# Kernel tuning notes

Measured on AMD Instinct MI355X. Metric: run time of the kernel, lower is better.

Reference implementation:

```python
import jax, jax.numpy as jnp
import numpy as np

B, LQ, LKV, D = 32, 1024, 1024, 512

def setup_inputs() -> dict:
    key = jax.random.key(0)
    kq, kkv = jax.random.split(key)
    query = jax.random.normal(kq, (B, LQ, D), dtype=jnp.float32)
    key_value = jax.random.normal(kkv, (B, LKV, D), dtype=jnp.float32)
    return {"query": query, "key_value": key_value}

def reference(query, key_value):
    # scores: [B, Lq, Lkv] (unscaled dot-product attention)
    scores = jnp.einsum('bqd,bkd->bqk', query, key_value)
    attn_score = jax.nn.softmax(scores, axis=-1)
    # output: [B, Lq, D]
    output = jnp.einsum('bqk,bkd->bqd', attn_score, key_value)
    return (output, attn_score)
```

## Files before the change

kernel.cpp:

```cpp
#include <hip/hip_runtime.h>


constexpr int NB  = 32;
constexpr int LQ  = 1024;
constexpr int LKV = 1024;
constexpr int DD  = 512;
constexpr int NROWS = NB * LQ;

typedef __attribute__((ext_vector_type(4))) float f4;
typedef __attribute__((ext_vector_type(4))) float f32x4;
typedef __attribute__((ext_vector_type(4))) unsigned short u16x4;
typedef __attribute__((ext_vector_type(8))) __bf16 bf16x8;

__device__ __forceinline__ unsigned short f2bf(float x) {
  unsigned u = __builtin_bit_cast(unsigned, x);
  unsigned r = u + 0x7FFFu + ((u >> 16) & 1u);
  return (unsigned short)(r >> 16);
}
__device__ __forceinline__ float bf2f(unsigned short h) {
  unsigned u = ((unsigned)h) << 16;
  return __builtin_bit_cast(float, u);
}

__device__ __forceinline__ void gload16(const void* g, void* l) {
  __builtin_amdgcn_global_load_lds((const __attribute__((address_space(1))) unsigned int*)g,
                                   (__attribute__((address_space(3))) unsigned int*)l,
                                   16, 0, 0);
}

constexpr int PAD = 40;

__global__ __launch_bounds__(256) void prep_all_kernel(const float* __restrict__ Q,
                                                       const float* __restrict__ KV,
                                                       unsigned short* __restrict__ Qh,
                                                       unsigned short* __restrict__ Ql,
                                                       unsigned short* __restrict__ Kh,
                                                       unsigned short* __restrict__ Kl,
                                                       unsigned short* __restrict__ KVT)
{
  __shared__ unsigned short T[64][72];
  const int b  = blockIdx.z;
  const int tk = blockIdx.y;
  const int td = blockIdx.x;
  const int tid = threadIdx.x;

#pragma unroll
  for (int i = 0; i < 4; ++i) {
    int idx = tid + i * 256;
    int r   = idx >> 4;
    int c4  = (idx & 15) << 2;
    size_t goff = ((size_t)b * LKV + tk * 64 + r) * DD + td * 64 + c4;
    f4 v = *(const f4*)(KV + goff);
    u16x4 h, l;
#pragma unroll
    for (int u = 0; u < 4; ++u) {
      h[u] = f2bf(v[u]);
      l[u] = f2bf(v[u] - bf2f(h[u]));
    }
    *(u16x4*)&T[r][c4] = h;
    *(u16x4*)(Kh + goff) = h;
    *(u16x4*)(Kl + goff) = l;

    f4 q = *(const f4*)(Q + goff);
    u16x4 qh, ql;
#pragma unroll
    for (int u = 0; u < 4; ++u) {
      qh[u] = f2bf(q[u]);
      ql[u] = f2bf(q[u] - bf2f(qh[u]));
    }
    *(u16x4*)(Qh + goff) = qh;
    *(u16x4*)(Ql + goff) = ql;
  }
  __syncthreads();

#pragma unroll
  for (int i = 0; i < 4; ++i) {
    int idx = tid + i * 256;
    int c   = idx >> 4;
    int r4  = (idx & 15) << 2;
    u16x4 w = { T[r4][c], T[r4 + 1][c], T[r4 + 2][c], T[r4 + 3][c] };
    *(u16x4*)(KVT + ((size_t)b * DD + td * 64 + c) * LKV + tk * 64 + r4) = w;
  }
}

__global__ __launch_bounds__(256) void gemm_qk4_kernel(const unsigned short* __restrict__ Qh,
                                                       const unsigned short* __restrict__ Ql,
                                                       const unsigned short* __restrict__ Kh,
                                                       const unsigned short* __restrict__ Kl,
                                                       float* __restrict__ S,
                                                       float* __restrict__ Pmax,
                                                       float* __restrict__ Psum)
{
  __shared__ unsigned short SM[4][128 * 64];
  const int b   = blockIdx.y;
  const int ti  = blockIdx.x >> 3;
  const int tj  = blockIdx.x & 7;
  const int tid  = threadIdx.x;
  const int lane = tid & 63;
  const int wid  = tid >> 6;
  const int wr = (wid >> 1) * 64;
  const int wc = (wid & 1) * 64;

  const size_t qo = ((size_t)b * LQ  + ti * 128) * DD;
  const size_t ko = ((size_t)b * LKV + tj * 128) * DD;
  const unsigned short* tb =
      (wid == 0) ? Qh + qo : (wid == 1) ? Ql + qo : (wid == 2) ? Kh + ko : Kl + ko;

  const int lrow = lane >> 3;
  const int ss   = (lane & 7) ^ lrow;

  f32x4 acc[4][4] = {};

  for (int ks = 0; ks < DD; ks += 64) {
    __syncthreads();
#pragma unroll
    for (int i = 0; i < 16; ++i) {
      const unsigned short* g = tb + (size_t)(i * 8 + lrow) * DD + ks + ss * 8;
      gload16(g, &SM[wid][i * 512]);
    }
    __syncthreads();

#pragma unroll
    for (int kk = 0; kk < 64; kk += 32) {
      const int cl  = (kk + ((lane >> 4) << 3)) >> 3;
      const int sp8 = (cl ^ (lane & 7)) * 8;
      bf16x8 ah[4], al[4], bh[4], bl[4];
#pragma unroll
      for (int m = 0; m < 4; ++m) {
        int r = wr + m * 16 + (lane & 15);
        ah[m] = *(const bf16x8*)&SM[0][r * 64 + sp8];
        al[m] = *(const bf16x8*)&SM[1][r * 64 + sp8];
      }
#pragma unroll
      for (int n = 0; n < 4; ++n) {
        int r = wc + n * 16 + (lane & 15);
        bh[n] = *(const bf16x8*)&SM[2][r * 64 + sp8];
        bl[n] = *(const bf16x8*)&SM[3][r * 64 + sp8];
      }
#pragma unroll
      for (int m = 0; m < 4; ++m)
#pragma unroll
        for (int n = 0; n < 4; ++n)
          acc[m][n] = __builtin_amdgcn_mfma_f32_16x16x32_bf16(ah[m], bh[n], acc[m][n], 0, 0, 0);
#pragma unroll
      for (int m = 0; m < 4; ++m)
#pragma unroll
        for (int n = 0; n < 4; ++n)
          acc[m][n] = __builtin_amdgcn_mfma_f32_16x16x32_bf16(ah[m], bl[n], acc[m][n], 0, 0, 0);
#pragma unroll
      for (int m = 0; m < 4; ++m)
#pragma unroll
        for (int n = 0; n < 4; ++n)
          acc[m][n] = __builtin_amdgcn_mfma_f32_16x16x32_bf16(al[m], bh[n], acc[m][n], 0, 0, 0);
    }
  }

  float* Sb = S + (size_t)b * LQ * LKV;
#pragma unroll
  for (int m = 0; m < 4; ++m) {
    int row0 = ti * 128 + wr + m * 16 + ((lane >> 4) << 2);
#pragma unroll
    for (int n = 0; n < 4; ++n) {
      int col = tj * 128 + wc + n * 16 + (lane & 15);
#pragma unroll
      for (int j = 0; j < 4; ++j)
        Sb[(size_t)(row0 + j) * LKV + col] = acc[m][n][j];
    }
  }

  const int g16  = lane >> 4;
  const int l16  = lane & 15;
  const int wcid = wc >> 6;
#pragma unroll
  for (int m = 0; m < 4; ++m) {
#pragma unroll
    for (int j = 0; j < 4; ++j) {
      float rm = fmaxf(fmaxf(acc[m][0][j], acc[m][1][j]), fmaxf(acc[m][2][j], acc[m][3][j]));
#pragma unroll
      for (int off = 8; off >= 1; off >>= 1)
        rm = fmaxf(rm, __shfl_xor(rm, off));
      float se = 0.f;
#pragma unroll
      for (int n = 0; n < 4; ++n)
        se += __expf(acc[m][n][j] - rm);
#pragma unroll
      for (int off = 8; off >= 1; off >>= 1)
        se += __shfl_xor(se, off);
      if (l16 == 0) {
        int row  = ti * 128 + wr + m * 16 + g16 * 4 + j;
        size_t p = ((size_t)b * LQ + row) * 16 + tj * 2 + wcid;
        Pmax[p] = rm;
        Psum[p] = se;
      }
    }
  }
}

__global__ __launch_bounds__(256) void reduce_stats_kernel(const float* __restrict__ Pmax,
                                                           const float* __restrict__ Psum,
                                                           float* __restrict__ M,
                                                           float* __restrict__ Inv)
{
  int row = blockIdx.x * 256 + threadIdx.x;
  const float* pm = Pmax + (size_t)row * 16;
  const float* ps = Psum + (size_t)row * 16;
  float mx = pm[0];
#pragma unroll
  for (int i = 1; i < 16; ++i) mx = fmaxf(mx, pm[i]);
  float s = 0.f;
#pragma unroll
  for (int i = 0; i < 16; ++i) s += ps[i] * __expf(pm[i] - mx);
  M[row]   = mx;
  Inv[row] = 1.0f / s;
}

__global__ __launch_bounds__(1024, 4) void gemm_av7_kernel(float* __restrict__ Sio,
                                                           const unsigned short* __restrict__ KVT,
                                                           const float* __restrict__ Mrow,
                                                           const float* __restrict__ Invr,
                                                           float* __restrict__ O)
{
  __shared__ unsigned short Asm[128][72];
  __shared__ unsigned short Bsm[512 * 64];
  __shared__ float Ms[128], Is[128];
  const int b  = blockIdx.y;
  const int mi = blockIdx.x;
  const int tid  = threadIdx.x;
  const int lane = tid & 63;
  const int wid  = tid >> 6;
  const int wr  = (wid >> 2) * 32;
  const int wcb = (wid & 3) * 128;

  float* Sb = Sio + ((size_t)b * LQ + mi * 128) * LKV;
  const unsigned short* Bb = KVT + (size_t)b * DD * LKV;

  if (tid < 128) {
    int gr = b * LQ + mi * 128 + tid;
    Ms[tid] = Mrow[gr];
    Is[tid] = Invr[gr];
  }

  const int lr8 = lane >> 3;
  const int ssw = (lane & 7) ^ lr8;

  f32x4 acc[2][8] = {};

  for (int ks = 0; ks < LKV; ks += 64) {
    __syncthreads();
#pragma unroll
    for (int i = 0; i < 2; ++i) {
      int idx = tid + i * 1024;
      int r   = idx >> 4;
      int k4  = (idx & 15) << 2;
      float* ap = Sb + (size_t)r * LKV + ks + k4;
      f4 v = *(const f4*)ap;
      float mr = Ms[r], ir = Is[r];
      f4 p; u16x4 h;
#pragma unroll
      for (int u = 0; u < 4; ++u) {
        p[u] = __expf(v[u] - mr) * ir;
        h[u] = f2bf(p[u]);
      }
      *(f4*)ap = p;
      *(u16x4*)&Asm[r][k4] = h;
    }
#pragma unroll
    for (int c = 0; c < 4; ++c) {
      int cc = wid * 4 + c;
      int dd = cc * 8 + lr8;
      const unsigned short* g = Bb + (size_t)dd * LKV + ks + ssw * 8;
      gload16(g, &Bsm[cc * 512]);
    }
    __syncthreads();

#pragma unroll
    for (int kk = 0; kk < 64; kk += 32) {
      const int kf = kk + ((lane >> 4) << 3);
      const int cl = kf >> 3;
      bf16x8 af[2];
#pragma unroll
      for (int m = 0; m < 2; ++m)
        af[m] = *(const bf16x8*)&Asm[wr + m * 16 + (lane & 15)][kf];
#pragma unroll
      for (int h = 0; h < 2; ++h) {
        bf16x8 bfv[4];
#pragma unroll
        for (int nn = 0; nn < 4; ++nn) {
          int dd = wcb + (h * 4 + nn) * 16 + (lane & 15);
          int sp = cl ^ (dd & 7);
          bfv[nn] = *(const bf16x8*)&Bsm[dd * 64 + sp * 8];
        }
#pragma unroll
        for (int m = 0; m < 2; ++m)
#pragma unroll
          for (int nn = 0; nn < 4; ++nn)
            acc[m][h * 4 + nn] =
                __builtin_amdgcn_mfma_f32_16x16x32_bf16(af[m], bfv[nn], acc[m][h * 4 + nn], 0, 0, 0);
      }
    }
  }

  float* Ob = O + ((size_t)b * LQ + mi * 128) * DD;
#pragma unroll
  for (int m = 0; m < 2; ++m) {
    int r0 = wr + m * 16 + ((lane >> 4) << 2);
#pragma unroll
    for (int n = 0; n < 8; ++n) {
      int col = wcb + n * 16 + (lane & 15);
#pragma unroll
      for (int j = 0; j < 4; ++j)
        Ob[(size_t)(r0 + j) * DD + col] = acc[m][n][j];
    }
  }
}

__global__ __launch_bounds__(256) void gemm_qk_kernel(const float* __restrict__ Q,
                                                      const float* __restrict__ KV,
                                                      float* __restrict__ S)
{
  __shared__ unsigned short Ah[128][PAD], Al[128][PAD], Bh[128][PAD], Bl[128][PAD];
  const int b   = blockIdx.y;
  const int ti  = blockIdx.x >> 3;
  const int tj  = blockIdx.x & 7;
  const int tid  = threadIdx.x;
  const int lane = tid & 63;
  const int wid  = tid >> 6;
  const int wr = (wid >> 1) * 64;
  const int wc = (wid & 1) * 64;

  const float* Qb = Q  + (size_t)b * LQ  * DD + (size_t)ti * 128 * DD;
  const float* Kb = KV + (size_t)b * LKV * DD + (size_t)tj * 128 * DD;

  f32x4 acc[4][4] = {};

  for (int ks = 0; ks < DD; ks += 32) {
    __syncthreads();
#pragma unroll
    for (int i = 0; i < 4; ++i) {
      int idx = tid + i * 256;
      int r   = idx >> 3;
      int k4  = (idx & 7) << 2;
      f4 qa = *(const f4*)(Qb + (size_t)r * DD + ks + k4);
      f4 ka = *(const f4*)(Kb + (size_t)r * DD + ks + k4);
      u16x4 qh, ql, kh, kl;
#pragma unroll
      for (int u = 0; u < 4; ++u) {
        unsigned short h = f2bf(qa[u]);
        qh[u] = h;  ql[u] = f2bf(qa[u] - bf2f(h));
        unsigned short h2 = f2bf(ka[u]);
        kh[u] = h2; kl[u] = f2bf(ka[u] - bf2f(h2));
      }
      *(u16x4*)&Ah[r][k4] = qh;  *(u16x4*)&Al[r][k4] = ql;
      *(u16x4*)&Bh[r][k4] = kh;  *(u16x4*)&Bl[r][k4] = kl;
    }
    __syncthreads();

    const int kf = (lane >> 4) << 3;
    bf16x8 ah[4], al[4], bh[4], bl[4];
#pragma unroll
    for (int m = 0; m < 4; ++m) {
      int row = wr + m * 16 + (lane & 15);
      ah[m] = *(const bf16x8*)&Ah[row][kf];
      al[m] = *(const bf16x8*)&Al[row][kf];
    }
#pragma unroll
    for (int n = 0; n < 4; ++n) {
      int row = wc + n * 16 + (lane & 15);
      bh[n] = *(const bf16x8*)&Bh[row][kf];
      bl[n] = *(const bf16x8*)&Bl[row][kf];
    }
#pragma unroll
    for (int m = 0; m < 4; ++m)
#pragma unroll
      for (int n = 0; n < 4; ++n) {
        acc[m][n] = __builtin_amdgcn_mfma_f32_16x16x32_bf16(ah[m], bh[n], acc[m][n], 0, 0, 0);
        acc[m][n] = __builtin_amdgcn_mfma_f32_16x16x32_bf16(ah[m], bl[n], acc[m][n], 0, 0, 0);
        acc[m][n] = __builtin_amdgcn_mfma_f32_16x16x32_bf16(al[m], bh[n], acc[m][n], 0, 0, 0);
      }
  }

  float* Sb = S + (size_t)b * LQ * LKV;
#pragma unroll
  for (int m = 0; m < 4; ++m) {
    int row0 = ti * 128 + wr + m * 16 + ((lane >> 4) << 2);
#pragma unroll
    for (int n = 0; n < 4; ++n) {
      int col = tj * 128 + wc + n * 16 + (lane & 15);
#pragma unroll
      for (int j = 0; j < 4; ++j)
        Sb[(size_t)(row0 + j) * LKV + col] = acc[m][n][j];
    }
  }
}

__global__ __launch_bounds__(256) void softmax_kernel(float* __restrict__ S)
{
  __shared__ float redmax[4], redsum[4];
  const int tid = threadIdx.x;
  float* p = S + (size_t)blockIdx.x * LKV;

  f4 v = *(const f4*)(p + tid * 4);
  float mx = fmaxf(fmaxf(v[0], v[1]), fmaxf(v[2], v[3]));
#pragma unroll
  for (int off = 32; off >= 1; off >>= 1)
    mx = fmaxf(mx, __shfl_xor(mx, off));
  if ((tid & 63) == 0) redmax[tid >> 6] = mx;
  __syncthreads();
  mx = fmaxf(fmaxf(redmax[0], redmax[1]), fmaxf(redmax[2], redmax[3]));

  f4 e;
#pragma unroll
  for (int u = 0; u < 4; ++u) e[u] = __expf(v[u] - mx);
  float sm = e[0] + e[1] + e[2] + e[3];
#pragma unroll
  for (int off = 32; off >= 1; off >>= 1)
    sm += __shfl_xor(sm, off);
  if ((tid & 63) == 0) redsum[tid >> 6] = sm;
  __syncthreads();
  sm = redsum[0] + redsum[1] + redsum[2] + redsum[3];

  float inv = 1.0f / sm;
  f4 o = { e[0] * inv, e[1] * inv, e[2] * inv, e[3] * inv };
  *(f4*)(p + tid * 4) = o;
}

__global__ __launch_bounds__(256) void kvt_prep_kernel(const float* __restrict__ KV,
                                                       unsigned short* __restrict__ KVT)
{
  __shared__ unsigned short T[64][72];
  const int b  = blockIdx.z;
  const int tk = blockIdx.y;
  const int td = blockIdx.x;
  const int tid = threadIdx.x;

#pragma unroll
  for (int i = 0; i < 4; ++i) {
    int idx = tid + i * 256;
    int r   = idx >> 4;
    int c4  = (idx & 15) << 2;
    f4 v = *(const f4*)(KV + ((size_t)b * LKV + tk * 64 + r) * DD + td * 64 + c4);
    u16x4 h;
#pragma unroll
    for (int u = 0; u < 4; ++u) h[u] = f2bf(v[u]);
    *(u16x4*)&T[r][c4] = h;
  }
  __syncthreads();

#pragma unroll
  for (int i = 0; i < 4; ++i) {
    int idx = tid + i * 256;
    int c   = idx >> 4;
    int r4  = (idx & 15) << 2;
    u16x4 w = { T[r4][c], T[r4 + 1][c], T[r4 + 2][c], T[r4 + 3][c] };
    *(u16x4*)(KVT + ((size_t)b * DD + td * 64 + c) * LKV + tk * 64 + r4) = w;
  }
}

__global__ __launch_bounds__(512) void gemm_av2_kernel(const float* __restrict__ A,
                                                       const unsigned short* __restrict__ KVT,
                                                       float* __restrict__ O)
{
  __shared__ unsigned short Asm[128][72];
  __shared__ unsigned short Bsm[256 * 64];
  const int b  = blockIdx.z;
  const int mi = blockIdx.y;
  const int nj = blockIdx.x;
  const int tid  = threadIdx.x;
  const int lane = tid & 63;
  const int wid  = tid >> 6;
  const int wr = (wid >> 2) * 64;
  const int wc = (wid & 3) * 64;

  const float* Ab = A + (size_t)b * LQ * LKV + (size_t)mi * 128 * LKV;
  const unsigned short* Bb = KVT + ((size_t)b * DD + nj * 256) * LKV;

  f32x4 acc[4][4] = {};

  for (int ks = 0; ks < LKV; ks += 64) {
    __syncthreads();
#pragma unroll
    for (int i = 0; i < 4; ++i) {
      int idx = tid + i * 512;
      int r   = idx >> 4;
      int k4  = (idx & 15) << 2;
      f4 v = *(const f4*)(Ab + (size_t)r * LKV + ks + k4);
      u16x4 h;
#pragma unroll
      for (int u = 0; u < 4; ++u) h[u] = f2bf(v[u]);
      *(u16x4*)&Asm[r][k4] = h;
    }
#pragma unroll
    for (int c = 0; c < 4; ++c) {
      int cc = wid * 4 + c;
      int dd = cc * 8 + (lane >> 3);
      int ss = (lane & 7) ^ (dd & 7);
      const unsigned short* g = Bb + (size_t)dd * LKV + ks + ss * 8;
      gload16(g, &Bsm[cc * 512]);
    }
    __syncthreads();

#pragma unroll
    for (int kk = 0; kk < 64; kk += 32) {
      const int kf = kk + ((lane >> 4) << 3);
      const int cl = kf >> 3;
      bf16x8 af[4], bfv[4];
#pragma unroll
      for (int m = 0; m < 4; ++m)
        af[m] = *(const bf16x8*)&Asm[wr + m * 16 + (lane & 15)][kf];
#pragma unroll
      for (int n = 0; n < 4; ++n) {
        int dd = wc + n * 16 + (lane & 15);
        int sp = cl ^ (dd & 7);
        bfv[n] = *(const bf16x8*)&Bsm[dd * 64 + sp * 8];
      }
#pragma unroll
      for (int m = 0; m < 4; ++m)
#pragma unroll
        for (int n = 0; n < 4; ++n)
          acc[m][n] = __builtin_amdgcn_mfma_f32_16x16x32_bf16(af[m], bfv[n], acc[m][n], 0, 0, 0);
    }
  }

  float* Ob = O + (size_t)b * LQ * DD;
#pragma unroll
  for (int m = 0; m < 4; ++m) {
    int row0 = mi * 128 + wr + m * 16 + ((lane >> 4) << 2);
#pragma unroll
    for (int n = 0; n < 4; ++n) {
      int col = nj * 256 + wc + n * 16 + (lane & 15);
#pragma unroll
      for (int j = 0; j < 4; ++j)
        Ob[(size_t)(row0 + j) * DD + col] = acc[m][n][j];
    }
  }
}

__global__ __launch_bounds__(256) void gemm_av_kernel(const float* __restrict__ A,
                                                      const float* __restrict__ KV,
                                                      float* __restrict__ O)
{
  __shared__ unsigned short Ab[128][PAD], Bt[128][PAD];
  const int b  = blockIdx.z;
  const int mi = blockIdx.y;
  const int nj = blockIdx.x;
  const int tid  = threadIdx.x;
  const int lane = tid & 63;
  const int wid  = tid >> 6;
  const int wr = (wid >> 1) * 64;
  const int wc = (wid & 1) * 64;

  const float* Arow = A  + (size_t)b * LQ * LKV + (size_t)mi * 128 * LKV;
  const float* Kb   = KV + (size_t)b * LKV * DD;

  f32x4 acc[4][4] = {};

  for (int ks = 0; ks < LKV; ks += 32) {
    __syncthreads();
#pragma unroll
    for (int i = 0; i < 4; ++i) {
      int idx = tid + i * 256;
      {
        int r  = idx >> 3;
        int k4 = (idx & 7) << 2;
        f4 av = *(const f4*)(Arow + (size_t)r * LKV + ks + k4);
        u16x4 h;
#pragma unroll
        for (int u = 0; u < 4; ++u) h[u] = f2bf(av[u]);
        *(u16x4*)&Ab[r][k4] = h;
      }
      {
        int kr = idx >> 5;
        int c4 = (idx & 31) << 2;
        f4 kv = *(const f4*)(Kb + (size_t)(ks + kr) * DD + nj * 128 + c4);
        unsigned short hv[4];
#pragma unroll
        for (int u = 0; u < 4; ++u) hv[u] = f2bf(kv[u]);
#pragma unroll
        for (int u = 0; u < 4; ++u) {
          int uu = (u + kr) & 3;
          Bt[c4 + uu][kr] = hv[uu];
        }
      }
    }
    __syncthreads();

    const int kf = (lane >> 4) << 3;
    bf16x8 af[4], bfv[4];
#pragma unroll
    for (int m = 0; m < 4; ++m)
      af[m] = *(const bf16x8*)&Ab[wr + m * 16 + (lane & 15)][kf];
#pragma unroll
    for (int n = 0; n < 4; ++n)
      bfv[n] = *(const bf16x8*)&Bt[wc + n * 16 + (lane & 15)][kf];
#pragma unroll
    for (int m = 0; m < 4; ++m)
#pragma unroll
      for (int n = 0; n < 4; ++n)
        acc[m][n] = __builtin_amdgcn_mfma_f32_16x16x32_bf16(af[m], bfv[n], acc[m][n], 0, 0, 0);
  }

  float* Ob = O + (size_t)b * LQ * DD;
#pragma unroll
  for (int m = 0; m < 4; ++m) {
    int row0 = mi * 128 + wr + m * 16 + ((lane >> 4) << 2);
#pragma unroll
    for (int n = 0; n < 4; ++n) {
      int col = nj * 128 + wc + n * 16 + (lane & 15);
#pragma unroll
      for (int j = 0; j < 4; ++j)
        Ob[(size_t)(row0 + j) * DD + col] = acc[m][n][j];
    }
  }
}

extern "C" void kernel_launch(void* const* d_in, const int* in_sizes, int n_in,
                              void* d_out, int out_size, void* d_ws, size_t ws_size,
                              hipStream_t stream) {
  const float* Q  = (const float*)d_in[0];
  const float* KV = (const float*)d_in[1];
  float* out  = (float*)d_out;
  float* attn = out + (size_t)NB * LQ * DD;

  const size_t NQ  = (size_t)NB * LQ * DD;
  const size_t big_bytes = 5 * NQ * sizeof(unsigned short);
  const size_t kvt_bytes = NQ * sizeof(unsigned short);

  if (ws_size >= big_bytes) {
    unsigned short* Qh  = (unsigned short*)d_ws;
    unsigned short* Qlo = Qh  + NQ;
    unsigned short* Kh  = Qlo + NQ;
    unsigned short* Kl  = Kh  + NQ;
    unsigned short* KVT = Kl  + NQ;
    float* Pmax = out;
    float* Psum = out + (size_t)NROWS * 16;
    float* Mrow = (float*)Kh;
    float* Invr = Mrow + NROWS;

    prep_all_kernel<<<dim3(DD / 64, LKV / 64, NB), 256, 0, stream>>>(Q, KV, Qh, Qlo, Kh, Kl, KVT);
    gemm_qk4_kernel<<<dim3(64, NB), 256, 0, stream>>>(Qh, Qlo, Kh, Kl, attn, Pmax, Psum);
    reduce_stats_kernel<<<NROWS / 256, 256, 0, stream>>>(Pmax, Psum, Mrow, Invr);
    gemm_av7_kernel<<<dim3(LQ / 128, NB), 1024, 0, stream>>>(attn, KVT, Mrow, Invr, out);
  } else if (ws_size >= kvt_bytes) {
    unsigned short* KVT = (unsigned short*)d_ws;
    gemm_qk_kernel<<<dim3(64, NB), 256, 0, stream>>>(Q, KV, attn);
    kvt_prep_kernel<<<dim3(DD / 64, LKV / 64, NB), 256, 0, stream>>>(KV, KVT);
    softmax_kernel<<<dim3(NB * LQ), 256, 0, stream>>>(attn);
    gemm_av2_kernel<<<dim3(DD / 256, LQ / 128, NB), 512, 0, stream>>>(attn, KVT, out);
  } else {
    gemm_qk_kernel<<<dim3(64, NB), 256, 0, stream>>>(Q, KV, attn);
    softmax_kernel<<<dim3(NB * LQ), 256, 0, stream>>>(attn);
    gemm_av_kernel<<<dim3(DD / 128, LQ / 128, NB), 256, 0, stream>>>(attn, KV, out);
  }
}
```

Baseline: 297.8 us.

## Double-buffer LDS tiles in split-bf16 QK GEMM with 32-wide K steps

Rewrites the QK^T GEMM main loop to use two LDS buffers with a K-step of 32. The next slice is issued as global-to-LDS loads while MFMAs run on the current slice, leaving one barrier per iteration instead of two. The swizzle is adjusted for 32-column rows, and MFMA sections are wrapped in s_setprio. LDS footprint stays the same, but there are twice as many iterations, and the loads overlapping the MFMAs depend on the async load path.

```diff
diff --git a/kernel.cpp b/kernel.cpp
--- a/kernel.cpp
+++ b/kernel.cpp
@@ -83,7 +83,7 @@
   }
 }
 
-__global__ __launch_bounds__(256) void gemm_qk4_kernel(const unsigned short* __restrict__ Qh,
+__global__ __launch_bounds__(256) void gemm_qk5_kernel(const unsigned short* __restrict__ Qh,
                                                        const unsigned short* __restrict__ Ql,
                                                        const unsigned short* __restrict__ Kh,
                                                        const unsigned short* __restrict__ Kl,
@@ -91,7 +91,7 @@
                                                        float* __restrict__ Pmax,
                                                        float* __restrict__ Psum)
 {
-  __shared__ unsigned short SM[4][128 * 64];
+  __shared__ unsigned short SM[2][4][128 * 32];
   const int b   = blockIdx.y;
   const int ti  = blockIdx.x >> 3;
   const int tj  = blockIdx.x & 7;
@@ -106,53 +106,65 @@
   const unsigned short* tb =
       (wid == 0) ? Qh + qo : (wid == 1) ? Ql + qo : (wid == 2) ? Kh + ko : Kl + ko;
 
-  const int lrow = lane >> 3;
-  const int ss   = (lane & 7) ^ lrow;
+  const int lr  = lane >> 2;
+  const int ssw = (lane & 3) ^ ((lr >> 1) & 3);
 
   f32x4 acc[4][4] = {};
 
-  for (int ks = 0; ks < DD; ks += 64) {
-    __syncthreads();
-#pragma unroll
-    for (int i = 0; i < 16; ++i) {
-      const unsigned short* g = tb + (size_t)(i * 8 + lrow) * DD + ks + ss * 8;
-      gload16(g, &SM[wid][i * 512]);
-    }
-    __syncthreads();
-
-#pragma unroll
-    for (int kk = 0; kk < 64; kk += 32) {
-      const int cl  = (kk + ((lane >> 4) << 3)) >> 3;
-      const int sp8 = (cl ^ (lane & 7)) * 8;
-      bf16x8 ah[4], al[4], bh[4], bl[4];
-#pragma unroll
-      for (int m = 0; m < 4; ++m) {
-        int r = wr + m * 16 + (lane & 15);
-        ah[m] = *(const bf16x8*)&SM[0][r * 64 + sp8];
-        al[m] = *(const bf16x8*)&SM[1][r * 64 + sp8];
-      }
-#pragma unroll
-      for (int n = 0; n < 4; ++n) {
-        int r = wc + n * 16 + (lane & 15);
-        bh[n] = *(const bf16x8*)&SM[2][r * 64 + sp8];
-        bl[n] = *(const bf16x8*)&SM[3][r * 64 + sp8];
-      }
-#pragma unroll
-      for (int m = 0; m < 4; ++m)
-#pragma unroll
-        for (int n = 0; n < 4; ++n)
-          acc[m][n] = __builtin_amdgcn_mfma_f32_16x16x32_bf16(ah[m], bh[n], acc[m][n], 0, 0, 0);
-#pragma unroll
-      for (int m = 0; m < 4; ++m)
-#pragma unroll
-        for (int n = 0; n < 4; ++n)
-          acc[m][n] = __builtin_amdgcn_mfma_f32_16x16x32_bf16(ah[m], bl[n], acc[m][n], 0, 0, 0);
-#pragma unroll
-      for (int m = 0; m < 4; ++m)
-#pragma unroll
-        for (int n = 0; n < 4; ++n)
-          acc[m][n] = __builtin_amdgcn_mfma_f32_16x16x32_bf16(al[m], bh[n], acc[m][n], 0, 0, 0);
-    }
+#pragma unroll
+  for (int c = 0; c < 8; ++c) {
+    const unsigned short* g = tb + (size_t)(c * 16 + lr) * DD + 0 + ssw * 8;
+    gload16(g, &SM[0][wid][c * 512]);
+  }
+  __syncthreads();
+
+  const int l15 = lane & 15;
+  const int cl  = lane >> 4;
+  const int swz = (cl ^ ((l15 >> 1) & 3)) << 3;
+
+  for (int it = 0; it < 16; ++it) {
+    const int cur = it & 1;
+    if (it < 15) {
+      const int ks = (it + 1) * 32;
+#pragma unroll
+      for (int c = 0; c < 8; ++c) {
+        const unsigned short* g = tb + (size_t)(c * 16 + lr) * DD + ks + ssw * 8;
+        gload16(g, &SM[cur ^ 1][wid][c * 512]);
+      }
+    }
+    bf16x8 ah[4], al[4], bh[4], bl[4];
+#pragma unroll
+    for (int m = 0; m < 4; ++m) {
+      int rr = wr + m * 16 + l15;
+      int off = rr * 32 + swz;
+      ah[m] = *(const bf16x8*)&SM[cur][0][off];
+      al[m] = *(const bf16x8*)&SM[cur][1][off];
+    }
+#pragma unroll
+    for (int n = 0; n < 4; ++n) {
+      int rr = wc + n * 16 + l15;
+      int off = rr * 32 + swz;
+      bh[n] = *(const bf16x8*)&SM[cur][2][off];
+      bl[n] = *(const bf16x8*)&SM[cur][3][off];
+    }
+    __builtin_amdgcn_s_setprio(1);
+#pragma unroll
+    for (int m = 0; m < 4; ++m)
+#pragma unroll
+      for (int n = 0; n < 4; ++n)
+        acc[m][n] = __builtin_amdgcn_mfma_f32_16x16x32_bf16(ah[m], bh[n], acc[m][n], 0, 0, 0);
+#pragma unroll
+    for (int m = 0; m < 4; ++m)
+#pragma unroll
+      for (int n = 0; n < 4; ++n)
+        acc[m][n] = __builtin_amdgcn_mfma_f32_16x16x32_bf16(ah[m], bl[n], acc[m][n], 0, 0, 0);
+#pragma unroll
+    for (int m = 0; m < 4; ++m)
+#pragma unroll
+      for (int n = 0; n < 4; ++n)
+        acc[m][n] = __builtin_amdgcn_mfma_f32_16x16x32_bf16(al[m], bh[n], acc[m][n], 0, 0, 0);
+    __builtin_amdgcn_s_setprio(0);
+    __syncthreads();
   }
 
   float* Sb = S + (size_t)b * LQ * LKV;
@@ -637,7 +649,7 @@
     float* Invr = Mrow + NROWS;
 
     prep_all_kernel<<<dim3(DD / 64, LKV / 64, NB), 256, 0, stream>>>(Q, KV, Qh, Qlo, Kh, Kl, KVT);
-    gemm_qk4_kernel<<<dim3(64, NB), 256, 0, stream>>>(Qh, Qlo, Kh, Kl, attn, Pmax, Psum);
+    gemm_qk5_kernel<<<dim3(64, NB), 256, 0, stream>>>(Qh, Qlo, Kh, Kl, attn, Pmax, Psum);
     reduce_stats_kernel<<<NROWS / 256, 256, 0, stream>>>(Pmax, Psum, Mrow, Invr);
     gemm_av7_kernel<<<dim3(LQ / 128, NB), 1024, 0, stream>>>(attn, KVT, Mrow, Invr, out);
   } else if (ws_size >= kvt_bytes) {
```

New measurement: 315.1 us. 1.06x slower.
